# Kernel tuning notes

Hardware: AMD Instinct MI355X
Metric: run time of the kernel (lower is better)

The kernel has to match this reference:

```python
import jax, jax.numpy as jnp
import numpy as np

B, H, KVH, D, X = 16, 16, 4, 128, 4      # batch, q heads, kv heads, head dim, fp32 cache packing (X=16//elem_size)
BLK, MAXB = 16, 256                       # vllm block size, max kv blocks per seq (max_seqlen=4096)
NB = B * MAXB                             # total physical kv-cache blocks
MAX_NNZ = 64                              # max attended kv blocks per (head, query-block) row
LOCAL, STRIDE = 32, 8                     # local window (in vllm blocks) and vertical stride


def _build_layout():
    # Per-head CSR over vllm-block granularity: block kb attended by query block m iff
    # it is in the causal local window or on the head's stride phase.
    crow = np.zeros((H, MAXB + 1), np.int32)
    cols_per_head = []
    for h in range(H):
        cols = []
        for m in range(MAXB):
            ks = [kb for kb in range(m + 1) if (m - kb) < LOCAL or kb % STRIDE == h % STRIDE]
            ks = ks[-MAX_NNZ:]
            crow[h, m + 1] = crow[h, m] + len(ks)
            cols.extend(ks)
        cols_per_head.append(cols)
    maxlen = max(len(c) for c in cols_per_head)
    col = np.zeros((H, maxlen), np.int32)
    for h, c in enumerate(cols_per_head):
        col[h, :len(c)] = np.asarray(c, np.int32)
    return jnp.asarray(crow), jnp.asarray(col)


def setup_inputs() -> dict:
    key = jax.random.key(0)
    k1, k2, k3, k4 = jax.random.split(key, 4)
    q = jax.random.normal(k1, (B, H, D), dtype=jnp.float32)
    # vLLM paged caches: K [NB, KVH, D//X, BLK, X], V [NB, KVH, D, BLK]
    k_cache = jax.random.normal(k2, (NB, KVH, D // X, BLK, X), dtype=jnp.float32)
    v_cache = jax.random.normal(k3, (NB, KVH, D, BLK), dtype=jnp.float32)
    block_tables = jnp.arange(NB, dtype=jnp.int32).reshape(B, MAXB)
    context_lens = jax.random.randint(k4, (B,), 64, MAXB * BLK + 1).astype(jnp.int32)
    layout_crow, layout_col = _build_layout()
    return {"q": q, "k_cache": k_cache, "v_cache": v_cache,
            "block_tables": block_tables, "context_lens": context_lens,
            "layout_crow": layout_crow, "layout_col": layout_col}


def reference(q, k_cache, v_cache, block_tables, context_lens, layout_crow, layout_col):
    sm_scale = 1.0 / float(np.sqrt(D))
    q_pid = context_lens.astype(jnp.int32) - 1             # [B] decode-token position
    pbid = q_pid // BLK                                     # [B] query block row in CSR layout
    h_idx = jnp.arange(H)
    hkv = h_idx // (H // KVH)                               # kv head for each q head
    start = layout_crow[h_idx[None, :], pbid[:, None]]      # [B,H]
    end = layout_crow[h_idx[None, :], pbid[:, None] + 1]    # [B,H]
    j = jnp.arange(MAX_NNZ)
    idx = start[:, :, None] + j                             # [B,H,J]
    valid = idx < end[:, :, None]
    idx = jnp.clip(idx, 0, layout_col.shape[1] - 1)
    cols = layout_col[h_idx[None, :, None], idx]            # [B,H,J] logical kv block ids
    bt = block_tables[jnp.arange(B)[:, None, None], cols]   # [B,H,J] physical cache block ids
    # K block load mirrors the Triton pointer math: [D//X, BLK, X] -> [D//X, X, BLK] -> [D, BLK]
    kb = k_cache[bt, hkv[None, :, None]]                    # [B,H,J,D//X,BLK,X]
    kb = jnp.transpose(kb, (0, 1, 2, 3, 5, 4)).reshape(B, H, MAX_NNZ, D, BLK)
    vb = v_cache[bt, hkv[None, :, None]]                    # [B,H,J,D,BLK]
    scores = jnp.einsum('bhd,bhjdn->bhjn', q, kb) * sm_scale
    pos = cols[..., None] * BLK + jnp.arange(BLK)           # [B,H,J,BLK] absolute token positions
    mask = valid[..., None] & (pos <= q_pid[:, None, None, None])  # causal + block-validity
    scores = jnp.where(mask, scores, -jnp.inf)
    p = jax.nn.softmax(scores.reshape(B, H, -1), axis=-1).reshape(B, H, MAX_NNZ, BLK)
    out = jnp.einsum('bhjn,bhjdn->bhd', p, vb)              # [B,H,D]
    return out
```

## Files before the change

kernel.cpp:

```cpp
#include <hip/hip_runtime.h>
#include <math.h>

constexpr int B = 16, H = 16, KVH = 4, D = 128;
constexpr int BLK = 16, MAXB = 256;
constexpr int GRP = H / KVH;
constexpr int NSL = 32;
constexpr int WSTRIDE = D + 2;
constexpr int MAXCNT = 8;


__global__ __launch_bounds__(256) void sparse_attn_slice(
    const float* __restrict__ q,
    const float* __restrict__ k_cache,
    const float* __restrict__ v_cache,
    const int* __restrict__ block_tables,
    const int* __restrict__ context_lens,
    float* __restrict__ wsB)
{
    const int wg = blockIdx.x;
    const int gidx = wg >> 5;
    const int slice = wg & (NSL - 1);
    const int b = gidx >> 2, hkv = gidx & 3;
    const int tid = threadIdx.x;
    const int lane = tid & 63;
    const int wv = tid >> 6;

    const int q_pid = context_lens[b] - 1;
    const int pbid = q_pid >> 4;
    const int p = (hkv & 1) * 4;
    const int M = max(0, pbid - 31);
    int nstr = 0;
    #pragma unroll
    for (int u = 0; u < 4; ++u) {
        const int d = M - p - u;
        nstr += (d > 0) ? ((d + 7) >> 3) : 0;
    }
    const int U = nstr + (pbid - M + 1);
    const int cnt = (slice < U) ? ((U - 1 - slice) / NSL + 1) : 0;

    float* pb = wsB + (size_t)((gidx * NSL + slice) * GRP) * WSTRIDE;
    if (cnt == 0) {
        for (int i = tid; i < GRP * WSTRIDE; i += 256)
            pb[i] = ((i % WSTRIDE) == D) ? -INFINITY : 0.f;
        return;
    }

    __shared__ float s_q[GRP * D];
    __shared__ float s_p[GRP][MAXCNT * BLK];
    __shared__ int   s_col[MAXCNT], s_msk[MAXCNT], s_bt[MAXCNT];
    __shared__ float s_redm[GRP][4];
    __shared__ float s_reds[GRP];

    for (int i = tid; i < GRP * D; i += 256)
        s_q[i] = q[(b * H + hkv * GRP + (i >> 7)) * D + (i & 127)];
    if (tid < cnt) {
        const int i = slice + tid * NSL;
        int kb, mk;
        if (i < nstr) { kb = ((i >> 2) << 3) + p + (i & 3); mk = 1 << (i & 3); }
        else          { kb = M + (i - nstr);                mk = 15; }
        s_col[tid] = kb;
        s_msk[tid] = mk;
        s_bt[tid]  = block_tables[b * MAXB + kb];
    }
    __syncthreads();

    const float sm_scale = 0.08838834764831845f;

    const int n  = (lane >> 2) & 15;
    const int dq = lane & 3;
    float mx[GRP] = {-INFINITY, -INFINITY, -INFINITY, -INFINITY};
    for (int j = wv; j < cnt; j += 4) {
        const int pos = s_col[j] * BLK + n;
        float sc[GRP];
        if (pos <= q_pid) {
            const float4* kb = (const float4*)(k_cache + (size_t)(s_bt[j] * KVH + hkv) * (D * BLK));
            const float4* q4 = (const float4*)s_q;
            float acc[GRP] = {0.f, 0.f, 0.f, 0.f};
            #pragma unroll
            for (int i = 0; i < 8; ++i) {
                const int d1 = dq * 8 + i;
                const float4 kv = kb[d1 * 16 + n];
                #pragma unroll
                for (int g = 0; g < GRP; ++g) {
                    const float4 qv = q4[g * 32 + d1];
                    acc[g] += kv.x * qv.x + kv.y * qv.y + kv.z * qv.z + kv.w * qv.w;
                }
            }
            const int mk = s_msk[j];
            #pragma unroll
            for (int g = 0; g < GRP; ++g) {
                float a = acc[g];
                a += __shfl_xor(a, 1);
                a += __shfl_xor(a, 2);
                sc[g] = ((mk >> g) & 1) ? a * sm_scale : -INFINITY;
            }
        } else {
            #pragma unroll
            for (int g = 0; g < GRP; ++g) sc[g] = -INFINITY;
        }
        if (dq == 0) {
            #pragma unroll
            for (int g = 0; g < GRP; ++g) s_p[g][j * 16 + n] = sc[g];
        }
        #pragma unroll
        for (int g = 0; g < GRP; ++g) mx[g] = fmaxf(mx[g], sc[g]);
    }
    #pragma unroll
    for (int g = 0; g < GRP; ++g) {
        float v = mx[g];
        #pragma unroll
        for (int off = 1; off < 64; off <<= 1)
            v = fmaxf(v, __shfl_xor(v, off));
        if (lane == 0) s_redm[g][wv] = v;
    }
    __syncthreads();

    {
        const int g = wv;
        const float m = fmaxf(fmaxf(s_redm[g][0], s_redm[g][1]),
                              fmaxf(s_redm[g][2], s_redm[g][3]));
        float sum = 0.f;
        for (int e = lane; e < cnt * 16; e += 64) {
            const float v = s_p[g][e];
            const float pr = (v == -INFINITY) ? 0.f : __expf(v - m);
            s_p[g][e] = pr;
            sum += pr;
        }
        #pragma unroll
        for (int off = 1; off < 64; off <<= 1)
            sum += __shfl_xor(sum, off);
        if (lane == 0) { s_reds[g] = sum; s_redm[g][0] = m; }
    }
    __syncthreads();

    const int dd = tid >> 1;
    const int dh = tid & 1;
    float acc[GRP] = {0.f, 0.f, 0.f, 0.f};
    for (int jj = 0; jj < cnt; ++jj) {
        const float4* vb = (const float4*)(v_cache + (size_t)(s_bt[jj] * KVH + hkv) * (D * BLK));
        const float4 v0 = vb[tid * 2];
        const float4 v1 = vb[tid * 2 + 1];
        #pragma unroll
        for (int g = 0; g < GRP; ++g) {
            const float4 p0 = ((const float4*)s_p[g])[jj * 4 + dh * 2];
            const float4 p1 = ((const float4*)s_p[g])[jj * 4 + dh * 2 + 1];
            acc[g] += v0.x * p0.x + v0.y * p0.y + v0.z * p0.z + v0.w * p0.w
                    + v1.x * p1.x + v1.y * p1.y + v1.z * p1.z + v1.w * p1.w;
        }
    }
    #pragma unroll
    for (int g = 0; g < GRP; ++g)
        acc[g] += __shfl_xor(acc[g], 1);
    if (dh == 0) {
        #pragma unroll
        for (int g = 0; g < GRP; ++g)
            pb[g * WSTRIDE + dd] = acc[g];
    }
    if (tid == 0) {
        #pragma unroll
        for (int g = 0; g < GRP; ++g) {
            pb[g * WSTRIDE + D]     = s_redm[g][0];
            pb[g * WSTRIDE + D + 1] = s_reds[g];
        }
    }
}

__global__ __launch_bounds__(128) void sparse_attn_combine(
    const float* __restrict__ wsB,
    float* __restrict__ out)
{
    const int bh = blockIdx.x;
    const int h = bh & (H - 1);
    const int gidx = (bh >> 4) * 4 + (h >> 2);
    const int g = h & 3;
    const int d = threadIdx.x;

    const float* base = wsB + (size_t)(gidx * NSL * GRP + g) * WSTRIDE;

    float m = -INFINITY;
    #pragma unroll
    for (int s = 0; s < NSL; ++s)
        m = fmaxf(m, base[s * GRP * WSTRIDE + D]);

    float num = 0.f, den = 0.f;
    #pragma unroll
    for (int s = 0; s < NSL; ++s) {
        const float ms = base[s * GRP * WSTRIDE + D];
        const float ss = base[s * GRP * WSTRIDE + D + 1];
        const float a = (ms == -INFINITY) ? 0.f : __expf(ms - m);
        num += base[s * GRP * WSTRIDE + d] * a;
        den += ss * a;
    }
    out[bh * D + d] = num / den;
}

extern "C" void kernel_launch(void* const* d_in, const int* in_sizes, int n_in,
                              void* d_out, int out_size, void* d_ws, size_t ws_size,
                              hipStream_t stream) {
    const float* q            = (const float*)d_in[0];
    const float* k_cache      = (const float*)d_in[1];
    const float* v_cache      = (const float*)d_in[2];
    const int*   block_tables = (const int*)d_in[3];
    const int*   context_lens = (const int*)d_in[4];
    float* out = (float*)d_out;
    float* wsB = (float*)d_ws;

    sparse_attn_slice<<<B * KVH * NSL, 256, 0, stream>>>(
        q, k_cache, v_cache, block_tables, context_lens, wsB);
    sparse_attn_combine<<<B * H, 128, 0, stream>>>(wsB, out);
}
```

Before: 29.79 us.

## Switch slice kernel to per-wave online softmax with fused K/V processing

Each wave now processes its own KV blocks with an online-softmax update. Each wave loads the V block into registers before the QK dot product and accumulates P·V immediately. This removes the workgroup-wide max/sum barriers and the separate V pass. It also halves the slices per group (32 to 16) while writing one partial per wave, so the combine kernel now merges 64 partials per head instead of 32. The cost is more shuffle reductions per block and a larger workspace/combine read.

```diff
diff --git a/kernel.cpp b/kernel.cpp
--- a/kernel.cpp
+++ b/kernel.cpp
@@ -4,21 +4,22 @@
 constexpr int B = 16, H = 16, KVH = 4, D = 128;
 constexpr int BLK = 16, MAXB = 256;
 constexpr int GRP = H / KVH;
-constexpr int NSL = 32;
+constexpr int NSL = 16;
+constexpr int NE  = NSL * 4;
 constexpr int WSTRIDE = D + 2;
-constexpr int MAXCNT = 8;
+constexpr int ESTRIDE = GRP * WSTRIDE;
 
 
-__global__ __launch_bounds__(256) void sparse_attn_slice(
+__global__ __launch_bounds__(256) void sparse_attn_online(
     const float* __restrict__ q,
     const float* __restrict__ k_cache,
     const float* __restrict__ v_cache,
     const int* __restrict__ block_tables,
     const int* __restrict__ context_lens,
-    float* __restrict__ wsB)
+    float* __restrict__ ws)
 {
     const int wg = blockIdx.x;
-    const int gidx = wg >> 5;
+    const int gidx = wg >> 4;
     const int slice = wg & (NSL - 1);
     const int b = gidx >> 2, hkv = gidx & 3;
     const int tid = threadIdx.x;
@@ -32,163 +33,129 @@
     int nstr = 0;
     #pragma unroll
     for (int u = 0; u < 4; ++u) {
-        const int d = M - p - u;
-        nstr += (d > 0) ? ((d + 7) >> 3) : 0;
+        const int dd = M - p - u;
+        nstr += (dd > 0) ? ((dd + 7) >> 3) : 0;
     }
     const int U = nstr + (pbid - M + 1);
-    const int cnt = (slice < U) ? ((U - 1 - slice) / NSL + 1) : 0;
-
-    float* pb = wsB + (size_t)((gidx * NSL + slice) * GRP) * WSTRIDE;
-    if (cnt == 0) {
-        for (int i = tid; i < GRP * WSTRIDE; i += 256)
-            pb[i] = ((i % WSTRIDE) == D) ? -INFINITY : 0.f;
-        return;
-    }
 
     __shared__ float s_q[GRP * D];
-    __shared__ float s_p[GRP][MAXCNT * BLK];
-    __shared__ int   s_col[MAXCNT], s_msk[MAXCNT], s_bt[MAXCNT];
-    __shared__ float s_redm[GRP][4];
-    __shared__ float s_reds[GRP];
+    __shared__ float s_p[4][GRP][BLK];
 
     for (int i = tid; i < GRP * D; i += 256)
         s_q[i] = q[(b * H + hkv * GRP + (i >> 7)) * D + (i & 127)];
-    if (tid < cnt) {
-        const int i = slice + tid * NSL;
-        int kb, mk;
-        if (i < nstr) { kb = ((i >> 2) << 3) + p + (i & 3); mk = 1 << (i & 3); }
-        else          { kb = M + (i - nstr);                mk = 15; }
-        s_col[tid] = kb;
-        s_msk[tid] = mk;
-        s_bt[tid]  = block_tables[b * MAXB + kb];
-    }
     __syncthreads();
+    const float4* q4 = (const float4*)s_q;
 
     const float sm_scale = 0.08838834764831845f;
-
     const int n  = (lane >> 2) & 15;
     const int dq = lane & 3;
-    float mx[GRP] = {-INFINITY, -INFINITY, -INFINITY, -INFINITY};
-    for (int j = wv; j < cnt; j += 4) {
-        const int pos = s_col[j] * BLK + n;
-        float sc[GRP];
-        if (pos <= q_pid) {
-            const float4* kb = (const float4*)(k_cache + (size_t)(s_bt[j] * KVH + hkv) * (D * BLK));
-            const float4* q4 = (const float4*)s_q;
-            float acc[GRP] = {0.f, 0.f, 0.f, 0.f};
-            #pragma unroll
-            for (int i = 0; i < 8; ++i) {
-                const int d1 = dq * 8 + i;
-                const float4 kv = kb[d1 * 16 + n];
-                #pragma unroll
-                for (int g = 0; g < GRP; ++g) {
-                    const float4 qv = q4[g * 32 + d1];
-                    acc[g] += kv.x * qv.x + kv.y * qv.y + kv.z * qv.z + kv.w * qv.w;
-                }
-            }
-            const int mk = s_msk[j];
+
+    float m[GRP], s[GRP], o0[GRP], o1[GRP];
+    #pragma unroll
+    for (int g = 0; g < GRP; ++g) { m[g] = -INFINITY; s[g] = 0.f; o0[g] = 0.f; o1[g] = 0.f; }
+
+    for (int iu = slice + wv * NSL; iu < U; iu += 4 * NSL) {
+        int kb, mk;
+        if (iu < nstr) { kb = ((iu >> 2) << 3) + p + (iu & 3); mk = 1 << (iu & 3); }
+        else           { kb = M + (iu - nstr);                 mk = 15; }
+        const int bt = block_tables[b * MAXB + kb];
+        const float4* kp = (const float4*)(k_cache + (size_t)(bt * KVH + hkv) * (D * BLK));
+        const float4* vp = (const float4*)(v_cache + (size_t)(bt * KVH + hkv) * (D * BLK));
+
+        float4 vbuf[8];
+        #pragma unroll
+        for (int i = 0; i < 8; ++i) vbuf[i] = vp[lane * 8 + i];
+
+        const int pos = kb * BLK + n;
+        float acc[GRP] = {0.f, 0.f, 0.f, 0.f};
+        #pragma unroll
+        for (int i = 0; i < 8; ++i) {
+            const int d1 = dq * 8 + i;
+            const float4 kv = kp[d1 * 16 + n];
             #pragma unroll
             for (int g = 0; g < GRP; ++g) {
-                float a = acc[g];
-                a += __shfl_xor(a, 1);
-                a += __shfl_xor(a, 2);
-                sc[g] = ((mk >> g) & 1) ? a * sm_scale : -INFINITY;
+                const float4 qv = q4[g * 32 + d1];
+                acc[g] += kv.x * qv.x + kv.y * qv.y + kv.z * qv.z + kv.w * qv.w;
             }
-        } else {
+        }
+
+        #pragma unroll
+        for (int g = 0; g < GRP; ++g) {
+            float a = acc[g];
+            a += __shfl_xor(a, 1);
+            a += __shfl_xor(a, 2);
+            const float sc = (((mk >> g) & 1) && pos <= q_pid) ? a * sm_scale : -INFINITY;
+            float bm = sc;
             #pragma unroll
-            for (int g = 0; g < GRP; ++g) sc[g] = -INFINITY;
+            for (int off = 4; off < 64; off <<= 1)
+                bm = fmaxf(bm, __shfl_xor(bm, off));
+            const float mn = fmaxf(m[g], bm);
+            const float f = (m[g] == mn) ? 1.f : __expf(m[g] - mn);
+            const float pg = (sc == -INFINITY) ? 0.f : __expf(sc - mn);
+            float ps = pg;
+            #pragma unroll
+            for (int off = 4; off < 64; off <<= 1)
+                ps += __shfl_xor(ps, off);
+            s[g] = s[g] * f + ps;
+            o0[g] *= f; o1[g] *= f;
+            m[g] = mn;
+            if (dq == 0) s_p[wv][g][n] = pg;
         }
-        if (dq == 0) {
-            #pragma unroll
-            for (int g = 0; g < GRP; ++g) s_p[g][j * 16 + n] = sc[g];
+
+        #pragma unroll
+        for (int g = 0; g < GRP; ++g) {
+            const float4* pp = (const float4*)s_p[wv][g];
+            const float4 p0 = pp[0], p1 = pp[1], p2 = pp[2], p3 = pp[3];
+            o0[g] += vbuf[0].x*p0.x + vbuf[0].y*p0.y + vbuf[0].z*p0.z + vbuf[0].w*p0.w
+                   + vbuf[1].x*p1.x + vbuf[1].y*p1.y + vbuf[1].z*p1.z + vbuf[1].w*p1.w
+                   + vbuf[2].x*p2.x + vbuf[2].y*p2.y + vbuf[2].z*p2.z + vbuf[2].w*p2.w
+                   + vbuf[3].x*p3.x + vbuf[3].y*p3.y + vbuf[3].z*p3.z + vbuf[3].w*p3.w;
+            o1[g] += vbuf[4].x*p0.x + vbuf[4].y*p0.y + vbuf[4].z*p0.z + vbuf[4].w*p0.w
+                   + vbuf[5].x*p1.x + vbuf[5].y*p1.y + vbuf[5].z*p1.z + vbuf[5].w*p1.w
+                   + vbuf[6].x*p2.x + vbuf[6].y*p2.y + vbuf[6].z*p2.z + vbuf[6].w*p2.w
+                   + vbuf[7].x*p3.x + vbuf[7].y*p3.y + vbuf[7].z*p3.z + vbuf[7].w*p3.w;
         }
-        #pragma unroll
-        for (int g = 0; g < GRP; ++g) mx[g] = fmaxf(mx[g], sc[g]);
     }
+
+    float* pb = ws + (size_t)(wg * 4 + wv) * ESTRIDE;
     #pragma unroll
     for (int g = 0; g < GRP; ++g) {
-        float v = mx[g];
-        #pragma unroll
-        for (int off = 1; off < 64; off <<= 1)
-            v = fmaxf(v, __shfl_xor(v, off));
-        if (lane == 0) s_redm[g][wv] = v;
+        pb[g * WSTRIDE + 2 * lane]     = o0[g];
+        pb[g * WSTRIDE + 2 * lane + 1] = o1[g];
     }
-    __syncthreads();
-
-    {
-        const int g = wv;
-        const float m = fmaxf(fmaxf(s_redm[g][0], s_redm[g][1]),
-                              fmaxf(s_redm[g][2], s_redm[g][3]));
-        float sum = 0.f;
-        for (int e = lane; e < cnt * 16; e += 64) {
-            const float v = s_p[g][e];
-            const float pr = (v == -INFINITY) ? 0.f : __expf(v - m);
-            s_p[g][e] = pr;
-            sum += pr;
-        }
-        #pragma unroll
-        for (int off = 1; off < 64; off <<= 1)
-            sum += __shfl_xor(sum, off);
-        if (lane == 0) { s_reds[g] = sum; s_redm[g][0] = m; }
-    }
-    __syncthreads();
-
-    const int dd = tid >> 1;
-    const int dh = tid & 1;
-    float acc[GRP] = {0.f, 0.f, 0.f, 0.f};
-    for (int jj = 0; jj < cnt; ++jj) {
-        const float4* vb = (const float4*)(v_cache + (size_t)(s_bt[jj] * KVH + hkv) * (D * BLK));
-        const float4 v0 = vb[tid * 2];
-        const float4 v1 = vb[tid * 2 + 1];
+    if (lane == 0) {
         #pragma unroll
         for (int g = 0; g < GRP; ++g) {
-            const float4 p0 = ((const float4*)s_p[g])[jj * 4 + dh * 2];
-            const float4 p1 = ((const float4*)s_p[g])[jj * 4 + dh * 2 + 1];
-            acc[g] += v0.x * p0.x + v0.y * p0.y + v0.z * p0.z + v0.w * p0.w
-                    + v1.x * p1.x + v1.y * p1.y + v1.z * p1.z + v1.w * p1.w;
-        }
-    }
-    #pragma unroll
-    for (int g = 0; g < GRP; ++g)
-        acc[g] += __shfl_xor(acc[g], 1);
-    if (dh == 0) {
-        #pragma unroll
-        for (int g = 0; g < GRP; ++g)
-            pb[g * WSTRIDE + dd] = acc[g];
-    }
-    if (tid == 0) {
-        #pragma unroll
-        for (int g = 0; g < GRP; ++g) {
-            pb[g * WSTRIDE + D]     = s_redm[g][0];
-            pb[g * WSTRIDE + D + 1] = s_reds[g];
+            pb[g * WSTRIDE + D]     = m[g];
+            pb[g * WSTRIDE + D + 1] = s[g];
         }
     }
 }
 
 __global__ __launch_bounds__(128) void sparse_attn_combine(
-    const float* __restrict__ wsB,
+    const float* __restrict__ ws,
     float* __restrict__ out)
 {
     const int bh = blockIdx.x;
-    const int h = bh & (H - 1);
-    const int gidx = (bh >> 4) * 4 + (h >> 2);
+    const int h = bh & (H - 1), b = bh >> 4;
+    const int gidx = b * 4 + (h >> 2);
     const int g = h & 3;
     const int d = threadIdx.x;
 
-    const float* base = wsB + (size_t)(gidx * NSL * GRP + g) * WSTRIDE;
+    const float* base = ws + (size_t)gidx * NE * ESTRIDE + g * WSTRIDE;
 
     float m = -INFINITY;
-    #pragma unroll
-    for (int s = 0; s < NSL; ++s)
-        m = fmaxf(m, base[s * GRP * WSTRIDE + D]);
+    #pragma unroll 8
+    for (int e = 0; e < NE; ++e)
+        m = fmaxf(m, base[(size_t)e * ESTRIDE + D]);
 
     float num = 0.f, den = 0.f;
-    #pragma unroll
-    for (int s = 0; s < NSL; ++s) {
-        const float ms = base[s * GRP * WSTRIDE + D];
-        const float ss = base[s * GRP * WSTRIDE + D + 1];
+    #pragma unroll 4
+    for (int e = 0; e < NE; ++e) {
+        const float ms = base[(size_t)e * ESTRIDE + D];
+        const float ss = base[(size_t)e * ESTRIDE + D + 1];
         const float a = (ms == -INFINITY) ? 0.f : __expf(ms - m);
-        num += base[s * GRP * WSTRIDE + d] * a;
+        num += base[(size_t)e * ESTRIDE + d] * a;
         den += ss * a;
     }
     out[bh * D + d] = num / den;
@@ -203,9 +170,9 @@
     const int*   block_tables = (const int*)d_in[3];
     const int*   context_lens = (const int*)d_in[4];
     float* out = (float*)d_out;
-    float* wsB = (float*)d_ws;
+    float* ws  = (float*)d_ws;
 
-    sparse_attn_slice<<<B * KVH * NSL, 256, 0, stream>>>(
-        q, k_cache, v_cache, block_tables, context_lens, wsB);
-    sparse_attn_combine<<<B * H, 128, 0, stream>>>(wsB, out);
+    sparse_attn_online<<<B * KVH * NSL, 256, 0, stream>>>(
+        q, k_cache, v_cache, block_tables, context_lens, ws);
+    sparse_attn_combine<<<B * H, 128, 0, stream>>>(ws, out);
 }
```

Measured after the change: 64.82 us. 2.18x slower.

## Halve split-K slices and restructure QK/PV per-wave work with shared-memory reduction

Applied to the files above, without the earlier changes.

Cuts the number of KV slices per (batch, kv-head) from 32 to 16, so each workgroup handles up to 9 blocks. The QK stage now loads whole K blocks with fully coalesced float4 reads into registers and defers masking to the softmax pass. The PV stage splits blocks across waves and reduces partial outputs through shared memory, replacing the loop where all threads walk every block. The workspace layout is repacked per workgroup. This is meant to cut combine traffic and per-block overhead, at the cost of less parallelism and more shared memory and registers per workgroup.

```diff
diff --git a/kernel.cpp b/kernel.cpp
--- a/kernel.cpp
+++ b/kernel.cpp
@@ -4,22 +4,22 @@
 constexpr int B = 16, H = 16, KVH = 4, D = 128;
 constexpr int BLK = 16, MAXB = 256;
 constexpr int GRP = H / KVH;
-constexpr int NSL = 32;
-constexpr int WSTRIDE = D + 2;
-constexpr int MAXCNT = 8;
-
-
-__global__ __launch_bounds__(256) void sparse_attn_slice(
+constexpr int NSL = 16;
+constexpr int MAXCNT = 9;
+constexpr int OSZ = GRP * D;
+constexpr int WSTRIDE = OSZ + 2 * GRP;
+
+
+__global__ __launch_bounds__(256, 4) void sparse_attn_slice(
     const float* __restrict__ q,
     const float* __restrict__ k_cache,
     const float* __restrict__ v_cache,
     const int* __restrict__ block_tables,
     const int* __restrict__ context_lens,
-    float* __restrict__ wsB)
+    float* __restrict__ ws)
 {
     const int wg = blockIdx.x;
-    const int gidx = wg >> 5;
-    const int slice = wg & (NSL - 1);
+    const int gidx = wg >> 4, slice = wg & (NSL - 1);
     const int b = gidx >> 2, hkv = gidx & 3;
     const int tid = threadIdx.x;
     const int lane = tid & 63;
@@ -32,27 +32,27 @@
     int nstr = 0;
     #pragma unroll
     for (int u = 0; u < 4; ++u) {
-        const int d = M - p - u;
-        nstr += (d > 0) ? ((d + 7) >> 3) : 0;
+        const int dd = M - p - u;
+        nstr += (dd > 0) ? ((dd + 7) >> 3) : 0;
     }
     const int U = nstr + (pbid - M + 1);
     const int cnt = (slice < U) ? ((U - 1 - slice) / NSL + 1) : 0;
 
-    float* pb = wsB + (size_t)((gidx * NSL + slice) * GRP) * WSTRIDE;
+    float* pb = ws + (size_t)wg * WSTRIDE;
     if (cnt == 0) {
-        for (int i = tid; i < GRP * WSTRIDE; i += 256)
-            pb[i] = ((i % WSTRIDE) == D) ? -INFINITY : 0.f;
+        for (int i = tid; i < WSTRIDE; i += 256)
+            pb[i] = (i >= OSZ && i < OSZ + GRP) ? -INFINITY : 0.f;
         return;
     }
 
     __shared__ float s_q[GRP * D];
     __shared__ float s_p[GRP][MAXCNT * BLK];
     __shared__ int   s_col[MAXCNT], s_msk[MAXCNT], s_bt[MAXCNT];
-    __shared__ float s_redm[GRP][4];
-    __shared__ float s_reds[GRP];
-
-    for (int i = tid; i < GRP * D; i += 256)
-        s_q[i] = q[(b * H + hkv * GRP + (i >> 7)) * D + (i & 127)];
+    __shared__ float s_m[GRP], s_s[GRP];
+    __shared__ float s_o[4][GRP * D];
+
+    if (tid < 128)
+        ((float4*)s_q)[tid] = ((const float4*)(q + (size_t)(b * H + hkv * GRP) * D))[tid];
     if (tid < cnt) {
         const int i = slice + tid * NSL;
         int kb, mk;
@@ -65,130 +65,139 @@
     __syncthreads();
 
     const float sm_scale = 0.08838834764831845f;
-
-    const int n  = (lane >> 2) & 15;
-    const int dq = lane & 3;
-    float mx[GRP] = {-INFINITY, -INFINITY, -INFINITY, -INFINITY};
-    for (int j = wv; j < cnt; j += 4) {
-        const int pos = s_col[j] * BLK + n;
-        float sc[GRP];
-        if (pos <= q_pid) {
-            const float4* kb = (const float4*)(k_cache + (size_t)(s_bt[j] * KVH + hkv) * (D * BLK));
-            const float4* q4 = (const float4*)s_q;
+    const float4* q4 = (const float4*)s_q;
+
+    {
+        const int n = lane & 15;
+        const int dg = lane >> 4;
+        for (int j = wv; j < cnt; j += 4) {
+            const float4* kp = (const float4*)(k_cache + (size_t)(s_bt[j] * KVH + hkv) * (D * BLK));
+            float4 kb4[8];
+            #pragma unroll
+            for (int i = 0; i < 8; ++i) kb4[i] = kp[lane + 64 * i];
             float acc[GRP] = {0.f, 0.f, 0.f, 0.f};
             #pragma unroll
             for (int i = 0; i < 8; ++i) {
-                const int d1 = dq * 8 + i;
-                const float4 kv = kb[d1 * 16 + n];
+                const int d1 = dg + 4 * i;
+                const float4 kv = kb4[i];
                 #pragma unroll
                 for (int g = 0; g < GRP; ++g) {
                     const float4 qv = q4[g * 32 + d1];
                     acc[g] += kv.x * qv.x + kv.y * qv.y + kv.z * qv.z + kv.w * qv.w;
                 }
             }
-            const int mk = s_msk[j];
             #pragma unroll
             for (int g = 0; g < GRP; ++g) {
                 float a = acc[g];
-                a += __shfl_xor(a, 1);
-                a += __shfl_xor(a, 2);
-                sc[g] = ((mk >> g) & 1) ? a * sm_scale : -INFINITY;
-            }
-        } else {
-            #pragma unroll
-            for (int g = 0; g < GRP; ++g) sc[g] = -INFINITY;
-        }
-        if (dq == 0) {
-            #pragma unroll
-            for (int g = 0; g < GRP; ++g) s_p[g][j * 16 + n] = sc[g];
-        }
-        #pragma unroll
-        for (int g = 0; g < GRP; ++g) mx[g] = fmaxf(mx[g], sc[g]);
-    }
-    #pragma unroll
-    for (int g = 0; g < GRP; ++g) {
-        float v = mx[g];
+                a += __shfl_xor(a, 16);
+                a += __shfl_xor(a, 32);
+                if (dg == 0) s_p[g][j * 16 + n] = a * sm_scale;
+            }
+        }
+    }
+    __syncthreads();
+
+    {
+        const int g = wv;
+        const int tot = cnt * 16;
+        float vals[3];
+        float mx = -INFINITY;
+        #pragma unroll
+        for (int t = 0; t < 3; ++t) {
+            const int e = lane + 64 * t;
+            float v = -INFINITY;
+            if (e < tot) {
+                const int j = e >> 4, nn = e & 15;
+                const int pos = s_col[j] * BLK + nn;
+                if (((s_msk[j] >> g) & 1) && pos <= q_pid) v = s_p[g][e];
+            }
+            vals[t] = v;
+            mx = fmaxf(mx, v);
+        }
         #pragma unroll
         for (int off = 1; off < 64; off <<= 1)
-            v = fmaxf(v, __shfl_xor(v, off));
-        if (lane == 0) s_redm[g][wv] = v;
-    }
-    __syncthreads();
-
-    {
-        const int g = wv;
-        const float m = fmaxf(fmaxf(s_redm[g][0], s_redm[g][1]),
-                              fmaxf(s_redm[g][2], s_redm[g][3]));
+            mx = fmaxf(mx, __shfl_xor(mx, off));
         float sum = 0.f;
-        for (int e = lane; e < cnt * 16; e += 64) {
-            const float v = s_p[g][e];
-            const float pr = (v == -INFINITY) ? 0.f : __expf(v - m);
-            s_p[g][e] = pr;
-            sum += pr;
+        #pragma unroll
+        for (int t = 0; t < 3; ++t) {
+            const int e = lane + 64 * t;
+            const float pe = (vals[t] == -INFINITY) ? 0.f : __expf(vals[t] - mx);
+            sum += pe;
+            if (e < tot) s_p[g][e] = pe;
         }
         #pragma unroll
         for (int off = 1; off < 64; off <<= 1)
             sum += __shfl_xor(sum, off);
-        if (lane == 0) { s_reds[g] = sum; s_redm[g][0] = m; }
-    }
-    __syncthreads();
-
-    const int dd = tid >> 1;
-    const int dh = tid & 1;
-    float acc[GRP] = {0.f, 0.f, 0.f, 0.f};
-    for (int jj = 0; jj < cnt; ++jj) {
-        const float4* vb = (const float4*)(v_cache + (size_t)(s_bt[jj] * KVH + hkv) * (D * BLK));
-        const float4 v0 = vb[tid * 2];
-        const float4 v1 = vb[tid * 2 + 1];
+        if (lane == 0) { s_m[g] = mx; s_s[g] = sum; }
+    }
+    __syncthreads();
+
+    {
+        float o0[GRP] = {0.f, 0.f, 0.f, 0.f};
+        float o1[GRP] = {0.f, 0.f, 0.f, 0.f};
+        for (int j = wv; j < cnt; j += 4) {
+            const float4* vp = (const float4*)(v_cache + (size_t)(s_bt[j] * KVH + hkv) * (D * BLK));
+            float4 vb4[8];
+            #pragma unroll
+            for (int i = 0; i < 8; ++i) vb4[i] = vp[lane * 8 + i];
+            #pragma unroll
+            for (int g = 0; g < GRP; ++g) {
+                const float4* pp = (const float4*)&s_p[g][j * 16];
+                const float4 p0 = pp[0], p1 = pp[1], p2 = pp[2], p3 = pp[3];
+                o0[g] += vb4[0].x*p0.x + vb4[0].y*p0.y + vb4[0].z*p0.z + vb4[0].w*p0.w
+                       + vb4[1].x*p1.x + vb4[1].y*p1.y + vb4[1].z*p1.z + vb4[1].w*p1.w
+                       + vb4[2].x*p2.x + vb4[2].y*p2.y + vb4[2].z*p2.z + vb4[2].w*p2.w
+                       + vb4[3].x*p3.x + vb4[3].y*p3.y + vb4[3].z*p3.z + vb4[3].w*p3.w;
+                o1[g] += vb4[4].x*p0.x + vb4[4].y*p0.y + vb4[4].z*p0.z + vb4[4].w*p0.w
+                       + vb4[5].x*p1.x + vb4[5].y*p1.y + vb4[5].z*p1.z + vb4[5].w*p1.w
+                       + vb4[6].x*p2.x + vb4[6].y*p2.y + vb4[6].z*p2.z + vb4[6].w*p2.w
+                       + vb4[7].x*p3.x + vb4[7].y*p3.y + vb4[7].z*p3.z + vb4[7].w*p3.w;
+            }
+        }
         #pragma unroll
         for (int g = 0; g < GRP; ++g) {
-            const float4 p0 = ((const float4*)s_p[g])[jj * 4 + dh * 2];
-            const float4 p1 = ((const float4*)s_p[g])[jj * 4 + dh * 2 + 1];
-            acc[g] += v0.x * p0.x + v0.y * p0.y + v0.z * p0.z + v0.w * p0.w
-                    + v1.x * p1.x + v1.y * p1.y + v1.z * p1.z + v1.w * p1.w;
-        }
-    }
-    #pragma unroll
-    for (int g = 0; g < GRP; ++g)
-        acc[g] += __shfl_xor(acc[g], 1);
-    if (dh == 0) {
-        #pragma unroll
-        for (int g = 0; g < GRP; ++g)
-            pb[g * WSTRIDE + dd] = acc[g];
-    }
-    if (tid == 0) {
-        #pragma unroll
-        for (int g = 0; g < GRP; ++g) {
-            pb[g * WSTRIDE + D]     = s_redm[g][0];
-            pb[g * WSTRIDE + D + 1] = s_reds[g];
+            float2* dst = (float2*)&s_o[wv][g * D + 2 * lane];
+            *dst = make_float2(o0[g], o1[g]);
+        }
+    }
+    __syncthreads();
+
+    {
+        const int f = tid * 2;
+        const float r0 = s_o[0][f] + s_o[1][f] + s_o[2][f] + s_o[3][f];
+        const float r1 = s_o[0][f+1] + s_o[1][f+1] + s_o[2][f+1] + s_o[3][f+1];
+        ((float2*)pb)[tid] = make_float2(r0, r1);
+        if (tid < GRP) {
+            pb[OSZ + tid]       = s_m[tid];
+            pb[OSZ + GRP + tid] = s_s[tid];
         }
     }
 }
 
 __global__ __launch_bounds__(128) void sparse_attn_combine(
-    const float* __restrict__ wsB,
+    const float* __restrict__ ws,
     float* __restrict__ out)
 {
     const int bh = blockIdx.x;
-    const int h = bh & (H - 1);
-    const int gidx = (bh >> 4) * 4 + (h >> 2);
+    const int h = bh & (H - 1), b = bh >> 4;
+    const int gidx = b * KVH + (h >> 2);
     const int g = h & 3;
     const int d = threadIdx.x;
 
-    const float* base = wsB + (size_t)(gidx * NSL * GRP + g) * WSTRIDE;
+    const float* base = ws + (size_t)(gidx * NSL) * WSTRIDE;
 
     float m = -INFINITY;
     #pragma unroll
-    for (int s = 0; s < NSL; ++s)
-        m = fmaxf(m, base[s * GRP * WSTRIDE + D]);
+    for (int e = 0; e < NSL; ++e)
+        m = fmaxf(m, base[e * WSTRIDE + OSZ + g]);
 
     float num = 0.f, den = 0.f;
     #pragma unroll
-    for (int s = 0; s < NSL; ++s) {
-        const float ms = base[s * GRP * WSTRIDE + D];
-        const float ss = base[s * GRP * WSTRIDE + D + 1];
+    for (int e = 0; e < NSL; ++e) {
+        const float ms = base[e * WSTRIDE + OSZ + g];
+        const float ss = base[e * WSTRIDE + OSZ + GRP + g];
         const float a = (ms == -INFINITY) ? 0.f : __expf(ms - m);
-        num += base[s * GRP * WSTRIDE + d] * a;
+        num += base[e * WSTRIDE + g * D + d] * a;
         den += ss * a;
     }
     out[bh * D + d] = num / den;
@@ -203,9 +212,9 @@
     const int*   block_tables = (const int*)d_in[3];
     const int*   context_lens = (const int*)d_in[4];
     float* out = (float*)d_out;
-    float* wsB = (float*)d_ws;
+    float* ws  = (float*)d_ws;
 
     sparse_attn_slice<<<B * KVH * NSL, 256, 0, stream>>>(
-        q, k_cache, v_cache, block_tables, context_lens, wsB);
-    sparse_attn_combine<<<B * H, 128, 0, stream>>>(wsB, out);
+        q, k_cache, v_cache, block_tables, context_lens, ws);
+    sparse_attn_combine<<<B * H, 128, 0, stream>>>(ws, out);
 }
```

Measured after the change: 50.70 us. +70.2%, slower.

## Halve slice count and prefetch V blocks into registers before softmax

Applied to the files above, without the earlier changes.

Reduces the number of slices per (batch, kv-head) from 32 to 16, so each workgroup handles up to 9 kv blocks. All V blocks are loaded into registers with a fully unrolled loop issued before the softmax barrier, which overlaps V fetch latency with the reduction phase. Padding entries get a zero mask and zero probabilities so that fixed-trip loops stay correct. The q load is vectorised. The cost is more registers per thread (18 float4s for V), which can lower occupancy, and more serial work per workgroup.

```diff
diff --git a/kernel.cpp b/kernel.cpp
--- a/kernel.cpp
+++ b/kernel.cpp
@@ -4,9 +4,9 @@
 constexpr int B = 16, H = 16, KVH = 4, D = 128;
 constexpr int BLK = 16, MAXB = 256;
 constexpr int GRP = H / KVH;
-constexpr int NSL = 32;
+constexpr int NSL = 16;
+constexpr int MAXCNT = 9;
 constexpr int WSTRIDE = D + 2;
-constexpr int MAXCNT = 8;
 
 
 __global__ __launch_bounds__(256) void sparse_attn_slice(
@@ -18,8 +18,7 @@
     float* __restrict__ wsB)
 {
     const int wg = blockIdx.x;
-    const int gidx = wg >> 5;
-    const int slice = wg & (NSL - 1);
+    const int gidx = wg >> 4, slice = wg & (NSL - 1);
     const int b = gidx >> 2, hkv = gidx & 3;
     const int tid = threadIdx.x;
     const int lane = tid & 63;
@@ -32,8 +31,8 @@
     int nstr = 0;
     #pragma unroll
     for (int u = 0; u < 4; ++u) {
-        const int d = M - p - u;
-        nstr += (d > 0) ? ((d + 7) >> 3) : 0;
+        const int dd = M - p - u;
+        nstr += (dd > 0) ? ((dd + 7) >> 3) : 0;
     }
     const int U = nstr + (pbid - M + 1);
     const int cnt = (slice < U) ? ((U - 1 - slice) / NSL + 1) : 0;
@@ -49,118 +48,135 @@
     __shared__ float s_p[GRP][MAXCNT * BLK];
     __shared__ int   s_col[MAXCNT], s_msk[MAXCNT], s_bt[MAXCNT];
     __shared__ float s_redm[GRP][4];
-    __shared__ float s_reds[GRP];
-
-    for (int i = tid; i < GRP * D; i += 256)
-        s_q[i] = q[(b * H + hkv * GRP + (i >> 7)) * D + (i & 127)];
-    if (tid < cnt) {
-        const int i = slice + tid * NSL;
+    __shared__ float s_m[GRP], s_s[GRP];
+
+    if (tid < 128)
+        ((float4*)s_q)[tid] = ((const float4*)(q + (size_t)(b * H + hkv * GRP) * D))[tid];
+    if (tid < MAXCNT) {
+        const int i = min(slice + tid * NSL, U - 1);
         int kb, mk;
         if (i < nstr) { kb = ((i >> 2) << 3) + p + (i & 3); mk = 1 << (i & 3); }
         else          { kb = M + (i - nstr);                mk = 15; }
         s_col[tid] = kb;
-        s_msk[tid] = mk;
+        s_msk[tid] = (tid < cnt) ? mk : 0;
         s_bt[tid]  = block_tables[b * MAXB + kb];
     }
     __syncthreads();
 
     const float sm_scale = 0.08838834764831845f;
+    const float4* q4 = (const float4*)s_q;
 
     const int n  = (lane >> 2) & 15;
     const int dq = lane & 3;
-    float mx[GRP] = {-INFINITY, -INFINITY, -INFINITY, -INFINITY};
-    for (int j = wv; j < cnt; j += 4) {
-        const int pos = s_col[j] * BLK + n;
-        float sc[GRP];
-        if (pos <= q_pid) {
-            const float4* kb = (const float4*)(k_cache + (size_t)(s_bt[j] * KVH + hkv) * (D * BLK));
-            const float4* q4 = (const float4*)s_q;
-            float acc[GRP] = {0.f, 0.f, 0.f, 0.f};
-            #pragma unroll
-            for (int i = 0; i < 8; ++i) {
-                const int d1 = dq * 8 + i;
-                const float4 kv = kb[d1 * 16 + n];
+    {
+        float mx[GRP] = {-INFINITY, -INFINITY, -INFINITY, -INFINITY};
+        for (int j = wv; j < cnt; j += 4) {
+            const int pos = s_col[j] * BLK + n;
+            float sc[GRP];
+            if (pos <= q_pid) {
+                const float4* kp = (const float4*)(k_cache + (size_t)(s_bt[j] * KVH + hkv) * (D * BLK));
+                float acc[GRP] = {0.f, 0.f, 0.f, 0.f};
+                #pragma unroll
+                for (int i = 0; i < 8; ++i) {
+                    const int d1 = dq * 8 + i;
+                    const float4 kv = kp[d1 * 16 + n];
+                    #pragma unroll
+                    for (int g = 0; g < GRP; ++g) {
+                        const float4 qv = q4[g * 32 + d1];
+                        acc[g] += kv.x * qv.x + kv.y * qv.y + kv.z * qv.z + kv.w * qv.w;
+                    }
+                }
+                const int mk = s_msk[j];
                 #pragma unroll
                 for (int g = 0; g < GRP; ++g) {
-                    const float4 qv = q4[g * 32 + d1];
-                    acc[g] += kv.x * qv.x + kv.y * qv.y + kv.z * qv.z + kv.w * qv.w;
+                    float a = acc[g];
+                    a += __shfl_xor(a, 1);
+                    a += __shfl_xor(a, 2);
+                    sc[g] = ((mk >> g) & 1) ? a * sm_scale : -INFINITY;
                 }
-            }
-            const int mk = s_msk[j];
-            #pragma unroll
-            for (int g = 0; g < GRP; ++g) {
-                float a = acc[g];
-                a += __shfl_xor(a, 1);
-                a += __shfl_xor(a, 2);
-                sc[g] = ((mk >> g) & 1) ? a * sm_scale : -INFINITY;
-            }
-        } else {
-            #pragma unroll
-            for (int g = 0; g < GRP; ++g) sc[g] = -INFINITY;
-        }
-        if (dq == 0) {
-            #pragma unroll
-            for (int g = 0; g < GRP; ++g) s_p[g][j * 16 + n] = sc[g];
-        }
-        #pragma unroll
-        for (int g = 0; g < GRP; ++g) mx[g] = fmaxf(mx[g], sc[g]);
-    }
-    #pragma unroll
-    for (int g = 0; g < GRP; ++g) {
-        float v = mx[g];
-        #pragma unroll
-        for (int off = 1; off < 64; off <<= 1)
-            v = fmaxf(v, __shfl_xor(v, off));
-        if (lane == 0) s_redm[g][wv] = v;
+            } else {
+                #pragma unroll
+                for (int g = 0; g < GRP; ++g) sc[g] = -INFINITY;
+            }
+            if (dq == 0) {
+                #pragma unroll
+                for (int g = 0; g < GRP; ++g) s_p[g][j * 16 + n] = sc[g];
+            }
+            #pragma unroll
+            for (int g = 0; g < GRP; ++g) mx[g] = fmaxf(mx[g], sc[g]);
+        }
+        #pragma unroll
+        for (int g = 0; g < GRP; ++g) {
+            float v = mx[g];
+            #pragma unroll
+            for (int off = 1; off < 64; off <<= 1)
+                v = fmaxf(v, __shfl_xor(v, off));
+            if (lane == 0) s_redm[g][wv] = v;
+        }
+    }
+
+    float4 vr0[MAXCNT], vr1[MAXCNT];
+    #pragma unroll
+    for (int jj = 0; jj < MAXCNT; ++jj) {
+        const int jc = (jj < cnt) ? jj : cnt - 1;
+        const float4* vp = (const float4*)(v_cache + (size_t)(s_bt[jc] * KVH + hkv) * (D * BLK));
+        vr0[jj] = vp[tid * 2];
+        vr1[jj] = vp[tid * 2 + 1];
     }
     __syncthreads();
 
     {
         const int g = wv;
-        const float m = fmaxf(fmaxf(s_redm[g][0], s_redm[g][1]),
-                              fmaxf(s_redm[g][2], s_redm[g][3]));
+        const int tot = cnt * BLK;
+        const float mg = fmaxf(fmaxf(s_redm[g][0], s_redm[g][1]),
+                               fmaxf(s_redm[g][2], s_redm[g][3]));
         float sum = 0.f;
-        for (int e = lane; e < cnt * 16; e += 64) {
-            const float v = s_p[g][e];
-            const float pr = (v == -INFINITY) ? 0.f : __expf(v - m);
-            s_p[g][e] = pr;
-            sum += pr;
+        #pragma unroll
+        for (int t = 0; t < 3; ++t) {
+            const int e = lane + 64 * t;
+            float pe = 0.f;
+            if (e < tot) {
+                const float v = s_p[g][e];
+                pe = (v == -INFINITY) ? 0.f : __expf(v - mg);
+            }
+            if (e < MAXCNT * BLK) s_p[g][e] = pe;
+            sum += pe;
         }
         #pragma unroll
         for (int off = 1; off < 64; off <<= 1)
             sum += __shfl_xor(sum, off);
-        if (lane == 0) { s_reds[g] = sum; s_redm[g][0] = m; }
+        if (lane == 0) { s_m[g] = mg; s_s[g] = sum; }
     }
     __syncthreads();
 
-    const int dd = tid >> 1;
-    const int dh = tid & 1;
-    float acc[GRP] = {0.f, 0.f, 0.f, 0.f};
-    for (int jj = 0; jj < cnt; ++jj) {
-        const float4* vb = (const float4*)(v_cache + (size_t)(s_bt[jj] * KVH + hkv) * (D * BLK));
-        const float4 v0 = vb[tid * 2];
-        const float4 v1 = vb[tid * 2 + 1];
-        #pragma unroll
-        for (int g = 0; g < GRP; ++g) {
-            const float4 p0 = ((const float4*)s_p[g])[jj * 4 + dh * 2];
-            const float4 p1 = ((const float4*)s_p[g])[jj * 4 + dh * 2 + 1];
-            acc[g] += v0.x * p0.x + v0.y * p0.y + v0.z * p0.z + v0.w * p0.w
-                    + v1.x * p1.x + v1.y * p1.y + v1.z * p1.z + v1.w * p1.w;
-        }
-    }
-    #pragma unroll
-    for (int g = 0; g < GRP; ++g)
-        acc[g] += __shfl_xor(acc[g], 1);
-    if (dh == 0) {
+    {
+        const int dh = tid & 1;
+        float acc[GRP] = {0.f, 0.f, 0.f, 0.f};
+        #pragma unroll
+        for (int jj = 0; jj < MAXCNT; ++jj) {
+            const float4 v0 = vr0[jj], v1 = vr1[jj];
+            #pragma unroll
+            for (int g = 0; g < GRP; ++g) {
+                const float4 p0 = ((const float4*)&s_p[g][jj * BLK])[dh * 2];
+                const float4 p1 = ((const float4*)&s_p[g][jj * BLK])[dh * 2 + 1];
+                acc[g] += v0.x * p0.x + v0.y * p0.y + v0.z * p0.z + v0.w * p0.w
+                        + v1.x * p1.x + v1.y * p1.y + v1.z * p1.z + v1.w * p1.w;
+            }
+        }
         #pragma unroll
         for (int g = 0; g < GRP; ++g)
-            pb[g * WSTRIDE + dd] = acc[g];
-    }
-    if (tid == 0) {
-        #pragma unroll
-        for (int g = 0; g < GRP; ++g) {
-            pb[g * WSTRIDE + D]     = s_redm[g][0];
-            pb[g * WSTRIDE + D + 1] = s_reds[g];
+            acc[g] += __shfl_xor(acc[g], 1);
+        if (dh == 0) {
+            #pragma unroll
+            for (int g = 0; g < GRP; ++g)
+                pb[g * WSTRIDE + (tid >> 1)] = acc[g];
+        }
+        if (tid == 0) {
+            #pragma unroll
+            for (int g = 0; g < GRP; ++g) {
+                pb[g * WSTRIDE + D]     = s_m[g];
+                pb[g * WSTRIDE + D + 1] = s_s[g];
+            }
         }
     }
 }
```

New measurement: 26.86 us. -9.8%, faster.
